# Performance work log

Hardware: AMD Instinct MI355X
Metric: run time of the kernel (lower is better)

Reference implementation:

```python
import jax, jax.numpy as jnp
import numpy as np

N = 100_000   # nodes
E = 1_600_000 # message-passing edges
EA = 1_000_000 # aux edges for bilinear head
G = 512       # graphs in batch
F_IN = 16     # num_node_features (fixed in source)
H = 32        # hidden_dim (fixed in source)


def setup_inputs() -> dict:
    key = jax.random.key(0)
    ks = jax.random.split(key, 8)
    x = jax.random.normal(ks[0], (N, F_IN), jnp.float32)
    edge_index = jax.random.randint(ks[1], (2, E), 0, N, dtype=jnp.int32)
    edge_index_aux = jax.random.randint(ks[2], (2, EA), 0, N, dtype=jnp.int32)
    batch = jnp.sort(jax.random.randint(ks[3], (N,), 0, G, dtype=jnp.int32))
    W1 = jax.random.normal(ks[4], (F_IN, H), jnp.float32) / np.sqrt(F_IN)
    b1 = jnp.zeros((H,), jnp.float32)
    W2 = jax.random.normal(ks[5], (H, H), jnp.float32) / np.sqrt(H)
    b2 = jnp.zeros((H,), jnp.float32)
    Wr = jax.random.normal(ks[6], (H, 1), jnp.float32) / np.sqrt(H)
    br = jnp.zeros((1,), jnp.float32)
    Wbil = jax.random.normal(ks[7], (1, H, H), jnp.float32) / H
    bbil = jnp.zeros((1,), jnp.float32)
    return dict(x=x, edge_index=edge_index, edge_index_aux=edge_index_aux,
                batch=batch, W1=W1, b1=b1, W2=W2, b2=b2, Wr=Wr, br=br,
                Wbil=Wbil, bbil=bbil)


def gcn_conv(x, W, b, src, dst):
    # PyG GCNConv: x' = D^{-1/2}(A+I)D^{-1/2} (x W) + b, deg includes self-loop
    xw = x @ W                                                   # [N,H]
    deg = jax.ops.segment_sum(jnp.ones((src.shape[0],), x.dtype), dst,
                              num_segments=N) + 1.0              # +1 self-loop
    dinv = jax.lax.rsqrt(deg)                                    # [N]
    coef = dinv[src] * dinv[dst]                                 # [E]
    agg = jax.ops.segment_sum(xw[src] * coef[:, None], dst, num_segments=N)
    agg = agg + xw * (dinv * dinv)[:, None]                      # self-loop msg
    return agg + b


def reference(x, edge_index, edge_index_aux, batch,
              W1, b1, W2, b2, Wr, br, Wbil, bbil):
    src, dst = edge_index[0], edge_index[1]
    h = jax.nn.relu(gcn_conv(x, W1, b1, src, dst))
    h = gcn_conv(h, W2, b2, src, dst)
    # global_mean_pool over graph ids
    cnt = jax.ops.segment_sum(jnp.ones((N,), h.dtype), batch, num_segments=G)
    pooled = jax.ops.segment_sum(h, batch, num_segments=G) / jnp.maximum(cnt, 1.0)[:, None]
    reg_output = pooled @ Wr + br                                # [G,1]
    # Bilinear edge head: out_e = x1_e^T W x2_e + b
    h1 = h[edge_index_aux[0]]                                    # [EA,H]
    h2 = h[edge_index_aux[1]]                                    # [EA,H]
    edge_pred = jnp.einsum('ei,ij,ej->e', h1, Wbil[0], h2)[:, None] + bbil
    return reg_output, edge_pred
```

## Files before the change

kernel.cpp:

```cpp
#include <hip/hip_runtime.h>
#include <hip/hip_bf16.h>
#include <string.h>
#include <stdint.h>

typedef __hip_bfloat16 bf16;

#define FIN 16
#define H   32
#define PADW 64
#define NB  512
#define BINCAP 4096
#define NPBMAX 200
#define PSTRIDE 65
#define CHUNK 8192
#define SCAN_CHUNK 1024
#define MAXSEG 64
#define POOLBLK 256

__device__ __forceinline__ float b2f(bf16 v) { return __bfloat162float(v); }

__device__ __forceinline__ float loadf(const void* p, size_t i, int f32) {
    return f32 ? ((const float*)p)[i] : b2f(((const bf16*)p)[i]);
}
__device__ __forceinline__ void storef(void* p, size_t i, float v, int f32) {
    if (f32) ((float*)p)[i] = v;
    else     ((bf16*)p)[i] = __float2bfloat16(v);
}

__device__ __forceinline__ unsigned pack2(float lo, float hi) {
    bf16 a = __float2bfloat16(lo), b = __float2bfloat16(hi);
    unsigned short ua, ub;
    memcpy(&ua, &a, 2); memcpy(&ub, &b, 2);
    return ((unsigned)ub << 16) | (unsigned)ua;
}
__device__ __forceinline__ float f_lo(unsigned u) {
    union { unsigned i; float f; } v; v.i = u << 16; return v.f;
}
__device__ __forceinline__ float f_hi(unsigned u) {
    union { unsigned i; float f; } v; v.i = u & 0xffff0000u; return v.f;
}

__global__ void k_detect(const void* __restrict__ x, int nelem, int* __restrict__ flag,
                         float* __restrict__ zf, int nzf,
                         int* __restrict__ zi, int nzi) {
    for (int i = threadIdx.x; i < nzf; i += blockDim.x) zf[i] = 0.f;
    if (zi) for (int i = threadIdx.x; i < nzi; i += blockDim.x) zi[i] = 0;
    __shared__ int cntS;
    if (threadIdx.x == 0) cntS = 0;
    __syncthreads();
    int bad = 0;
    const bf16* p = (const bf16*)x;
    for (int i = threadIdx.x; i < nelem; i += blockDim.x) {
        float v = b2f(p[i]);
        float a = fabsf(v);
        if (isnan(v) || a > 1024.f || (v != 0.f && a < 1e-20f)) bad++;
    }
    atomicAdd(&cntS, bad);
    __syncthreads();
    if (threadIdx.x == 0) flag[0] = (cntS > 64) ? 1 : 0;
}

__global__ void __launch_bounds__(1024) k_p1(
        const int* __restrict__ src, const int* __restrict__ dst,
        int* __restrict__ bincur, unsigned* __restrict__ binbuf,
        int E, int npb) {
    __shared__ int hcnt[4][NB];
    __shared__ int hbase[NB];
    __shared__ int scur[NB];
    int tid = threadIdx.x;
    int grp = tid >> 8;
    int e0 = blockIdx.x * CHUNK;
    int nE = E - e0;
    if (nE > CHUNK) nE = CHUNK;
    for (int i = tid; i < 4 * NB; i += blockDim.x) ((int*)hcnt)[i] = 0;
    __syncthreads();
    for (int i = tid; i < nE; i += blockDim.x)
        atomicAdd(&hcnt[grp][dst[e0 + i] / npb], 1);
    __syncthreads();
    for (int i = tid; i < NB; i += blockDim.x) {
        int c = hcnt[0][i] + hcnt[1][i] + hcnt[2][i] + hcnt[3][i];
        hbase[i] = c ? atomicAdd(&bincur[i], c) : 0;
        scur[i] = 0;
    }
    __syncthreads();
    for (int i = tid; i < nE; i += blockDim.x) {
        int d = dst[e0 + i];
        int bin = d / npb;
        int pos = hbase[bin] + atomicAdd(&scur[bin], 1);
        if (pos < BINCAP)
            binbuf[(size_t)bin * BINCAP + pos] =
                ((unsigned)src[e0 + i] << 10) | (unsigned)(d - bin * npb);
    }
}

__global__ void __launch_bounds__(256) k_p2(
        const int* __restrict__ bincur, const unsigned* __restrict__ binbuf,
        int* __restrict__ csr, int* __restrict__ deg, float* __restrict__ dinv,
        int N, int npb) {
    __shared__ int cur[NPBMAX];
    __shared__ int psr[NPBMAX * PSTRIDE];
    int b = blockIdx.x;
    int base = b * npb;
    int nn = N - base;
    if (nn > npb) nn = npb;
    if (nn < 0) nn = 0;
    for (int i = threadIdx.x; i < nn; i += blockDim.x) cur[i] = 0;
    __syncthreads();
    int cnt = bincur[b];
    if (cnt > BINCAP) cnt = BINCAP;
    const unsigned* buf = binbuf + (size_t)b * BINCAP;
    for (int j = threadIdx.x; j < cnt; j += blockDim.x) {
        unsigned p = buf[j];
        int loc = (int)(p & 1023u);
        int s = (int)(p >> 10);
        int pos = atomicAdd(&cur[loc], 1);
        if (pos < PADW) psr[loc * PSTRIDE + pos] = s;
    }
    __syncthreads();
    int tot = nn * PADW;
    for (int idx = threadIdx.x; idx < tot; idx += blockDim.x) {
        int i = idx >> 6, p = idx & 63;
        int dg = cur[i];
        if (dg > PADW) dg = PADW;
        if (p < dg)
            csr[((size_t)(base + i) << 6) + p] = psr[i * PSTRIDE + p];
    }
    for (int i = threadIdx.x; i < nn; i += blockDim.x) {
        int dg = cur[i];
        deg[base + i] = dg;
        dinv[base + i] = rsqrtf((float)dg + 1.0f);
    }
}


__global__ void k_fillp(const int* __restrict__ src, const int* __restrict__ dst,
                        int* __restrict__ cursor, int* __restrict__ csr, int E) {
    int e = blockIdx.x * blockDim.x + threadIdx.x;
    if (e >= E) return;
    int d = dst[e];
    int pos = atomicAdd(&cursor[d], 1);
    if (pos < PADW) csr[((size_t)d << 6) + pos] = src[e];
}

__global__ void k_dinvi(const int* __restrict__ deg, float* __restrict__ dinv, int N) {
    int t = blockIdx.x * blockDim.x + threadIdx.x;
    if (t < N) dinv[t] = rsqrtf((float)deg[t] + 1.0f);
}

__global__ void k_gatherpb(const int* __restrict__ deg, const int* __restrict__ csr,
                           const float* __restrict__ dinv, const unsigned* __restrict__ xsb,
                           float2* __restrict__ agg, int N) {
    int t = blockIdx.x * blockDim.x + threadIdx.x;
    int d = t >> 4, j = t & 15;
    if (d >= N) return;
    int len = deg[d];
    if (len > PADW) len = PADW;
    const int* lst = csr + ((size_t)d << 6);
    unsigned u = xsb[(size_t)d * 16 + j];
    float a0 = f_lo(u), a1 = f_hi(u);
    float b0 = 0.f, b1 = 0.f;
    int k = 0;
    for (; k + 4 <= len; k += 4) {
        int4 s4 = *(const int4*)(lst + k);
        unsigned u0 = xsb[(size_t)s4.x * 16 + j];
        unsigned u1 = xsb[(size_t)s4.y * 16 + j];
        unsigned u2 = xsb[(size_t)s4.z * 16 + j];
        unsigned u3 = xsb[(size_t)s4.w * 16 + j];
        a0 += f_lo(u0); a1 += f_hi(u0);
        b0 += f_lo(u1); b1 += f_hi(u1);
        a0 += f_lo(u2); a1 += f_hi(u2);
        b0 += f_lo(u3); b1 += f_hi(u3);
    }
    for (; k < len; k++) {
        unsigned u2 = xsb[(size_t)lst[k] * 16 + j];
        a0 += f_lo(u2); a1 += f_hi(u2);
    }
    float dv = dinv[d];
    agg[(size_t)d * 16 + j] = make_float2((a0 + b0) * dv, (a1 + b1) * dv);
}


__global__ void __launch_bounds__(256) k_xw1v(
        const void* __restrict__ x, const void* __restrict__ W1,
        const float* __restrict__ dinv, const int* __restrict__ flag,
        unsigned* __restrict__ xsb, int N) {
    __shared__ float sW[FIN * H];
    __shared__ float sxx[16 * 17];
    int f32 = flag[0];
    for (int i = threadIdx.x; i < FIN * H; i += blockDim.x) sW[i] = loadf(W1, i, f32);
    __syncthreads();
    int t = blockIdx.x * blockDim.x + threadIdx.x;
    int n = t >> 4, j = t & 15, g = threadIdx.x >> 4;
    if (n < N) sxx[g * 17 + j] = loadf(x, (size_t)n * FIN + j, f32);
    __syncthreads();
    if (n >= N) return;
    float dv = dinv[n];
    float s0 = 0.f, s1 = 0.f;
    const float* xp = &sxx[g * 17];
#pragma unroll
    for (int i = 0; i < FIN; i++) {
        float xv = xp[i];
        s0 += xv * sW[i * H + 2 * j];
        s1 += xv * sW[i * H + 2 * j + 1];
    }
    xsb[(size_t)n * 16 + j] = pack2(s0 * dv, s1 * dv);
}

__global__ void __launch_bounds__(256) k_h1xw2v(
        const void* __restrict__ W2, const void* __restrict__ b1,
        const float* __restrict__ dinv, const int* __restrict__ flag,
        const float2* __restrict__ aggv, unsigned* __restrict__ xsb2, int N) {
    __shared__ float sW[H * H];
    __shared__ float sb[H];
    __shared__ float shh[16 * 33];
    int f32 = flag[0];
    for (int i = threadIdx.x; i < H * H; i += blockDim.x) sW[i] = loadf(W2, i, f32);
    if (threadIdx.x < H) sb[threadIdx.x] = loadf(b1, threadIdx.x, f32);
    __syncthreads();
    int t = blockIdx.x * blockDim.x + threadIdx.x;
    int n = t >> 4, j = t & 15, g = threadIdx.x >> 4;
    if (n < N) {
        float2 a = aggv[(size_t)n * 16 + j];
        float v0 = a.x + sb[2 * j], v1 = a.y + sb[2 * j + 1];
        shh[g * 33 + 2 * j]     = v0 > 0.f ? v0 : 0.f;
        shh[g * 33 + 2 * j + 1] = v1 > 0.f ? v1 : 0.f;
    }
    __syncthreads();
    if (n >= N) return;
    float dv = dinv[n];
    float s0 = 0.f, s1 = 0.f;
    const float* hp = &shh[g * 33];
#pragma unroll
    for (int i = 0; i < H; i++) {
        float hv = hp[i];
        s0 += hv * sW[i * H + 2 * j];
        s1 += hv * sW[i * H + 2 * j + 1];
    }
    xsb2[(size_t)n * 16 + j] = pack2(s0 * dv, s1 * dv);
}

__global__ void __launch_bounds__(512) k_poolhb(
        const void* __restrict__ b2v, const void* __restrict__ Wbil,
        const int* __restrict__ batch, const int* __restrict__ flag,
        const float* __restrict__ aggB, float* __restrict__ pooled,
        float* __restrict__ cnt, bf16* __restrict__ hb, bf16* __restrict__ gb,
        int N) {
    __shared__ float sW[H * H];
    __shared__ float sb[H];
    __shared__ float sh[POOLBLK][H];
    __shared__ int   sg[POOLBLK];
    __shared__ float spool[MAXSEG * H];
    __shared__ float scnt[MAXSEG];
    int f32 = flag[0];
    int tid = threadIdx.x;
    for (int i = tid; i < H * H; i += blockDim.x) sW[i] = loadf(Wbil, i, f32);
    if (tid < H) sb[tid] = loadf(b2v, tid, f32);
    int blk0 = blockIdx.x * POOLBLK;
    int nvalid = N - blk0;
    if (nvalid > POOLBLK) nvalid = POOLBLK;
    if (tid < nvalid) sg[tid] = batch[blk0 + tid];
    for (int i = tid; i < MAXSEG * H; i += blockDim.x) spool[i] = 0.f;
    if (tid < MAXSEG) scnt[tid] = 0.f;
    __syncthreads();
    int f = tid & 31, k = tid >> 5;
    for (int r = k; r < nvalid; r += 16) {
        float v = aggB[(size_t)(blk0 + r) * H + f] + sb[f];
        sh[r][f] = v;
        hb[(size_t)(blk0 + r) * H + f] = __float2bfloat16(v);
    }
    __syncthreads();
    int g0 = sg[0];
    int nseg = sg[nvalid - 1] - g0 + 1;
    if (nseg <= MAXSEG) {
        for (int r = k; r < nvalid; r += 16) {
            int gl = sg[r] - g0;
            atomicAdd(&spool[gl * H + f], sh[r][f]);
            if (f == 0) atomicAdd(&scnt[gl], 1.f);
        }
    } else {
        for (int r = k; r < nvalid; r += 16) {
            atomicAdd(&pooled[(size_t)sg[r] * H + f], sh[r][f]);
            if (f == 0) atomicAdd(&cnt[sg[r]], 1.f);
        }
    }
    for (int r = k; r < nvalid; r += 16) {
        float s = 0.f;
#pragma unroll
        for (int i = 0; i < H; i++) s += sh[r][i] * sW[i * H + f];
        gb[(size_t)(blk0 + r) * H + f] = __float2bfloat16(s);
    }
    if (nseg <= MAXSEG) {
        __syncthreads();
        for (int i = tid; i < nseg * H; i += blockDim.x)
            atomicAdd(&pooled[(size_t)(g0 + (i >> 5)) * H + (i & 31)], spool[i]);
        for (int i = tid; i < nseg; i += blockDim.x)
            atomicAdd(&cnt[g0 + i], scnt[i]);
    }
}


__global__ void k_degi(const int* __restrict__ dst, int* __restrict__ deg, int E) {
    int t = blockIdx.x * blockDim.x + threadIdx.x;
    if (t < E) atomicAdd(&deg[dst[t]], 1);
}

__global__ void k_scan1(const int* __restrict__ deg, int* __restrict__ partials, int N) {
    __shared__ int sd[256];
    int base = blockIdx.x * SCAN_CHUNK + threadIdx.x * 4;
    int s = 0;
#pragma unroll
    for (int k = 0; k < 4; k++) { int i = base + k; s += (i < N) ? deg[i] : 0; }
    sd[threadIdx.x] = s;
    __syncthreads();
    for (int off = 128; off > 0; off >>= 1) {
        if (threadIdx.x < off) sd[threadIdx.x] += sd[threadIdx.x + off];
        __syncthreads();
    }
    if (threadIdx.x == 0) partials[blockIdx.x] = sd[0];
}

__global__ void k_scan2(const int* __restrict__ partials, int* __restrict__ chunk_off, int B1) {
    __shared__ int sd[256];
    int t = threadIdx.x;
    int lv[4];
    int s = 0;
#pragma unroll
    for (int k = 0; k < 4; k++) { int i = t * 4 + k; lv[k] = (i < B1) ? partials[i] : 0; s += lv[k]; }
    sd[t] = s;
    __syncthreads();
    int inc = s;
    for (int off = 1; off < 256; off <<= 1) {
        int v = (t >= off) ? sd[t - off] : 0;
        __syncthreads();
        sd[t] += v;
        __syncthreads();
    }
    int run = sd[t] - inc;
#pragma unroll
    for (int k = 0; k < 4; k++) { int i = t * 4 + k; if (i < B1) chunk_off[i] = run; run += lv[k]; }
    if (t == 255) chunk_off[B1] = run;
}

__global__ void k_scan3(const int* __restrict__ deg, const int* __restrict__ chunk_off,
                        int* __restrict__ row_ptr, int* __restrict__ cursor,
                        int N, int E) {
    __shared__ int sd[256];
    int t = threadIdx.x;
    int base = blockIdx.x * SCAN_CHUNK + t * 4;
    int lv[4];
    int s = 0;
#pragma unroll
    for (int k = 0; k < 4; k++) { int i = base + k; lv[k] = (i < N) ? deg[i] : 0; s += lv[k]; }
    sd[t] = s;
    __syncthreads();
    int inc = s;
    for (int off = 1; off < 256; off <<= 1) {
        int v = (t >= off) ? sd[t - off] : 0;
        __syncthreads();
        sd[t] += v;
        __syncthreads();
    }
    int run = chunk_off[blockIdx.x] + sd[t] - inc;
#pragma unroll
    for (int k = 0; k < 4; k++) {
        int i = base + k;
        if (i < N) { row_ptr[i] = run; cursor[i] = run; }
        run += lv[k];
    }
    if (blockIdx.x == 0 && t == 0) row_ptr[N] = E;
}

__global__ void k_fill(const int* __restrict__ src, const int* __restrict__ dst,
                       int* __restrict__ cursor, int* __restrict__ csr, int E) {
    int e = blockIdx.x * blockDim.x + threadIdx.x;
    if (e >= E) return;
    int pos = atomicAdd(&cursor[dst[e]], 1);
    csr[pos] = src[e];
}

__global__ void k_gather(const int* __restrict__ row_ptr, const int* __restrict__ csr,
                         const float* __restrict__ dinv, const float* __restrict__ xs,
                         float* __restrict__ agg, int N) {
    int t = blockIdx.x * blockDim.x + threadIdx.x;
    int d = t >> 5, f = t & 31;
    if (d >= N) return;
    int beg = row_ptr[d], end = row_ptr[d + 1];
    float acc  = xs[(size_t)d * H + f];
    float acc2 = 0.f;
    int j = beg;
    for (; j + 1 < end; j += 2) {
        int s0 = csr[j], s1 = csr[j + 1];
        acc  += xs[(size_t)s0 * H + f];
        acc2 += xs[(size_t)s1 * H + f];
    }
    if (j < end) acc += xs[(size_t)csr[j] * H + f];
    agg[(size_t)d * H + f] = (acc + acc2) * dinv[d];
}

__global__ void k_xw1n(const void* __restrict__ x, const void* __restrict__ W1,
                       const float* __restrict__ dinv, const int* __restrict__ flag,
                       float* __restrict__ xs, int N) {
    __shared__ float sW[FIN * H];
    int f32 = flag[0];
    for (int i = threadIdx.x; i < FIN * H; i += blockDim.x) sW[i] = loadf(W1, i, f32);
    __syncthreads();
    int n = blockIdx.x * blockDim.x + threadIdx.x;
    if (n >= N) return;
    float xr[FIN];
#pragma unroll
    for (int i = 0; i < FIN; i++) xr[i] = loadf(x, (size_t)n * FIN + i, f32);
    float dv = dinv[n];
#pragma unroll
    for (int f = 0; f < H; f++) {
        float s = 0.f;
#pragma unroll
        for (int i = 0; i < FIN; i++) s += xr[i] * sW[i * H + f];
        xs[(size_t)n * H + f] = s * dv;
    }
}

__global__ void k_h1xw2n(const void* __restrict__ W2, const void* __restrict__ b1,
                         const float* __restrict__ dinv, const int* __restrict__ flag,
                         const float* __restrict__ agg, float* __restrict__ xs2, int N) {
    __shared__ float sW[H * H];
    __shared__ float sb[H];
    int f32 = flag[0];
    for (int i = threadIdx.x; i < H * H; i += blockDim.x) sW[i] = loadf(W2, i, f32);
    if (threadIdx.x < H) sb[threadIdx.x] = loadf(b1, threadIdx.x, f32);
    __syncthreads();
    int n = blockIdx.x * blockDim.x + threadIdx.x;
    if (n >= N) return;
    float hr[H];
#pragma unroll
    for (int f = 0; f < H; f++) {
        float v = agg[(size_t)n * H + f] + sb[f];
        hr[f] = v > 0.f ? v : 0.f;
    }
    float dv = dinv[n];
#pragma unroll
    for (int f = 0; f < H; f++) {
        float s = 0.f;
#pragma unroll
        for (int i = 0; i < H; i++) s += hr[i] * sW[i * H + f];
        xs2[(size_t)n * H + f] = s * dv;
    }
}


__global__ void k_degf(const int* __restrict__ dst, float* __restrict__ deg, int E) {
    int t = blockIdx.x * blockDim.x + threadIdx.x;
    if (t < E) atomicAdd(&deg[dst[t]], 1.0f);
}
__global__ void k_dinvf(float* __restrict__ deg, int N) {
    int t = blockIdx.x * blockDim.x + threadIdx.x;
    if (t < N) deg[t] = rsqrtf(deg[t] + 1.0f);
}
__global__ void k_xw1o(const void* __restrict__ x, const void* __restrict__ W1,
                       const float* __restrict__ dinv, const int* __restrict__ flag,
                       float* __restrict__ xw, float* __restrict__ agg, int N) {
    __shared__ float sW[FIN * H];
    int f32 = flag[0];
    for (int i = threadIdx.x; i < FIN * H; i += blockDim.x) sW[i] = loadf(W1, i, f32);
    __syncthreads();
    int n = blockIdx.x * blockDim.x + threadIdx.x;
    if (n >= N) return;
    float xr[FIN];
#pragma unroll
    for (int i = 0; i < FIN; i++) xr[i] = loadf(x, (size_t)n * FIN + i, f32);
    float dv = dinv[n], dv2 = dv * dv;
#pragma unroll
    for (int f = 0; f < H; f++) {
        float s = 0.f;
#pragma unroll
        for (int i = 0; i < FIN; i++) s += xr[i] * sW[i * H + f];
        xw[(size_t)n * H + f]  = s;
        agg[(size_t)n * H + f] = s * dv2;
    }
}
__global__ void k_scatter(const int* __restrict__ src, const int* __restrict__ dst,
                          const float* __restrict__ dinv, const float* __restrict__ xw,
                          float* __restrict__ agg, int E) {
    int t = blockIdx.x * blockDim.x + threadIdx.x;
    int e = t >> 5, f = t & 31;
    if (e >= E) return;
    int s = src[e], d = dst[e];
    float c = dinv[s] * dinv[d];
    atomicAdd(&agg[(size_t)d * H + f], xw[(size_t)s * H + f] * c);
}
__global__ void k_h1xw2o(const void* __restrict__ W2, const void* __restrict__ b1,
                         const float* __restrict__ dinv, const int* __restrict__ flag,
                         float* __restrict__ aggio, float* __restrict__ xw2, int N) {
    __shared__ float sW[H * H];
    __shared__ float sb[H];
    int f32 = flag[0];
    for (int i = threadIdx.x; i < H * H; i += blockDim.x) sW[i] = loadf(W2, i, f32);
    if (threadIdx.x < H) sb[threadIdx.x] = loadf(b1, threadIdx.x, f32);
    __syncthreads();
    int n = blockIdx.x * blockDim.x + threadIdx.x;
    if (n >= N) return;
    float hr[H];
#pragma unroll
    for (int f = 0; f < H; f++) {
        float v = aggio[(size_t)n * H + f] + sb[f];
        hr[f] = v > 0.f ? v : 0.f;
    }
    float dv = dinv[n], dv2 = dv * dv;
#pragma unroll
    for (int f = 0; f < H; f++) {
        float s = 0.f;
#pragma unroll
        for (int i = 0; i < H; i++) s += hr[i] * sW[i * H + f];
        xw2[(size_t)n * H + f]   = s;
        aggio[(size_t)n * H + f] = s * dv2;
    }
}


__global__ void k_bilreg(const int* __restrict__ srcA, const int* __restrict__ dstA,
                         const unsigned* __restrict__ gb32, const unsigned* __restrict__ hb32,
                         const void* __restrict__ bbil,
                         const float* __restrict__ pooled, const float* __restrict__ cnt,
                         const void* __restrict__ Wr, const void* __restrict__ br,
                         const int* __restrict__ flag, void* __restrict__ out,
                         int G, int EA) {
    int f32 = flag[0];
    int t = blockIdx.x * blockDim.x + threadIdx.x;
    if (t < EA) {
        int s = srcA[t], d = dstA[t];
        const uint4* gp = (const uint4*)(gb32 + (size_t)s * (H / 2));
        const uint4* hp = (const uint4*)(hb32 + (size_t)d * (H / 2));
        float acc = 0.f;
#pragma unroll
        for (int kk = 0; kk < 4; kk++) {
            uint4 a = gp[kk], b = hp[kk];
            acc += f_lo(a.x) * f_lo(b.x) + f_hi(a.x) * f_hi(b.x);
            acc += f_lo(a.y) * f_lo(b.y) + f_hi(a.y) * f_hi(b.y);
            acc += f_lo(a.z) * f_lo(b.z) + f_hi(a.z) * f_hi(b.z);
            acc += f_lo(a.w) * f_lo(b.w) + f_hi(a.w) * f_hi(b.w);
        }
        storef(out, (size_t)G + t, acc + loadf(bbil, 0, f32), f32);
    } else {
        int g = t - EA;
        if (g < G) {
            float c = cnt[g];
            c = c > 1.f ? c : 1.f;
            float s = 0.f;
#pragma unroll
            for (int i = 0; i < H; i++) s += pooled[(size_t)g * H + i] * loadf(Wr, i, f32);
            storef(out, g, s / c + loadf(br, 0, f32), f32);
        }
    }
}

extern "C" void kernel_launch(void* const* d_in, const int* in_sizes, int n_in,
                              void* d_out, int out_size, void* d_ws, size_t ws_size,
                              hipStream_t stream) {
    const void* x     = d_in[0];
    const int*  ei    = (const int*)d_in[1];
    const int*  eia   = (const int*)d_in[2];
    const int*  batch = (const int*)d_in[3];
    const void* W1    = d_in[4];
    const void* b1    = d_in[5];
    const void* W2    = d_in[6];
    const void* b2    = d_in[7];
    const void* Wr    = d_in[8];
    const void* br    = d_in[9];
    const void* Wbil  = d_in[10];
    const void* bbil  = d_in[11];

    const int N  = in_sizes[0] / FIN;
    const int E  = in_sizes[1] / 2;
    const int EA = in_sizes[2] / 2;
    const int G  = out_size - EA;

    float* ws     = (float*)d_ws;
    int*   flag   = (int*)ws;
    float* dinv   = ws + 16;
    float* A      = dinv + N;
    float* B      = A + (size_t)N * H;
    float* pooled = B + (size_t)N * H;
    float* cnt    = pooled + (size_t)G * H;
    float* fend   = cnt + G;

    unsigned* xsb  = (unsigned*)A;
    unsigned* hb32 = (unsigned*)A;
    unsigned* gb32 = hb32 + (size_t)N * (H / 2);

    int* degA   = (int*)fend;
    int* csrA   = (int*)(((uintptr_t)(degA + N) + 15) & ~(uintptr_t)15);
    int* bincur = csrA + (size_t)N * PADW;
    size_t needA  = (size_t)((char*)bincur - (char*)d_ws);
    size_t needA2 = (size_t)((char*)(bincur + NB) - (char*)d_ws);
    const int B1 = (N + SCAN_CHUNK - 1) / SCAN_CHUNK;
    int* deg_i     = (int*)fend;
    int* curB      = deg_i + N;
    int* row_ptr   = curB + N;
    int* chunk_off = row_ptr + N + 1;
    int* csrB      = chunk_off + B1 + 1;
    size_t needB = (size_t)((char*)(csrB + E) - (char*)d_ws);

    const int npb = (N + NB - 1) / NB;
    const bool tierA2 = (ws_size >= needA2) && (npb <= NPBMAX) && (N <= (1 << 22)) &&
                        ((size_t)NB * BINCAP <= (size_t)N * H * 2);
    const bool tierA  = !tierA2 && (ws_size >= needA);
    const bool tierB  = !tierA2 && !tierA && (ws_size >= needB) && (B1 <= 1024);

    const int* src  = ei;
    const int* dst  = ei + E;
    const int* srcA = eia;
    const int* dstA = eia + EA;

    const int TB = 256;
    const int npool = G * H + G;

    k_detect<<<1, 1024, 0, stream>>>(x, 1024, flag, pooled, npool,
                                     tierA2 ? bincur : (int*)nullptr,
                                     tierA2 ? NB : 0);

    int ggrid16 = (int)(((long)N * 16 + TB - 1) / TB);
    int ggrid32 = (int)(((long)N * 32 + TB - 1) / TB);
    int ngrid   = (N + TB - 1) / TB;
    unsigned* xsb2 = xsb;
    float2* aggv = (float2*)B;

    if (tierA2) {
        unsigned* binbuf = (unsigned*)A;
        int nblk1 = (E + CHUNK - 1) / CHUNK;
        k_p1<<<nblk1, 1024, 0, stream>>>(src, dst, bincur, binbuf, E, npb);
        k_p2<<<NB, TB, 0, stream>>>(bincur, binbuf, csrA, degA, dinv, N, npb);
        k_xw1v<<<ggrid16, TB, 0, stream>>>(x, W1, dinv, flag, xsb, N);
        k_gatherpb<<<ggrid16, TB, 0, stream>>>(degA, csrA, dinv, xsb, aggv, N);
        k_h1xw2v<<<ggrid16, TB, 0, stream>>>(W2, b1, dinv, flag, aggv, xsb2, N);
        k_gatherpb<<<ggrid16, TB, 0, stream>>>(degA, csrA, dinv, xsb2, aggv, N);
    } else if (tierA) {
        hipMemsetAsync(degA, 0, (size_t)N * sizeof(int), stream);
        k_fillp<<<(E + TB - 1) / TB, TB, 0, stream>>>(src, dst, degA, csrA, E);
        k_dinvi<<<ngrid, TB, 0, stream>>>(degA, dinv, N);
        k_xw1v<<<ggrid16, TB, 0, stream>>>(x, W1, dinv, flag, xsb, N);
        k_gatherpb<<<ggrid16, TB, 0, stream>>>(degA, csrA, dinv, xsb, aggv, N);
        k_h1xw2v<<<ggrid16, TB, 0, stream>>>(W2, b1, dinv, flag, aggv, xsb2, N);
        k_gatherpb<<<ggrid16, TB, 0, stream>>>(degA, csrA, dinv, xsb2, aggv, N);
    } else if (tierB) {
        hipMemsetAsync(deg_i, 0, (size_t)N * sizeof(int), stream);
        k_degi<<<(E + TB - 1) / TB, TB, 0, stream>>>(dst, deg_i, E);
        k_dinvi<<<ngrid, TB, 0, stream>>>(deg_i, dinv, N);
        k_scan1<<<B1, TB, 0, stream>>>(deg_i, chunk_off, N);
        k_scan2<<<1, TB, 0, stream>>>(chunk_off, chunk_off, B1);
        k_scan3<<<B1, TB, 0, stream>>>(deg_i, chunk_off, row_ptr, curB, N, E);
        k_fill<<<(E + TB - 1) / TB, TB, 0, stream>>>(src, dst, curB, csrB, E);
        k_xw1n<<<ngrid, TB, 0, stream>>>(x, W1, dinv, flag, A, N);
        k_gather<<<ggrid32, TB, 0, stream>>>(row_ptr, csrB, dinv, A, B, N);
        k_h1xw2n<<<ngrid, TB, 0, stream>>>(W2, b1, dinv, flag, B, A, N);
        k_gather<<<ggrid32, TB, 0, stream>>>(row_ptr, csrB, dinv, A, B, N);
    } else {
        hipMemsetAsync(dinv, 0, (size_t)N * sizeof(float), stream);
        k_degf<<<(E + TB - 1) / TB, TB, 0, stream>>>(dst, dinv, E);
        k_dinvf<<<ngrid, TB, 0, stream>>>(dinv, N);
        k_xw1o<<<ngrid, TB, 0, stream>>>(x, W1, dinv, flag, A, B, N);
        long tot = (long)E * 32;
        int sgrid = (int)((tot + TB - 1) / TB);
        k_scatter<<<sgrid, TB, 0, stream>>>(src, dst, dinv, A, B, E);
        k_h1xw2o<<<ngrid, TB, 0, stream>>>(W2, b1, dinv, flag, B, A, N);
        k_scatter<<<sgrid, TB, 0, stream>>>(src, dst, dinv, A, B, E);
    }

    k_poolhb<<<(N + POOLBLK - 1) / POOLBLK, 512, 0, stream>>>(
        b2, Wbil, batch, flag, B, pooled, cnt, (bf16*)hb32, (bf16*)gb32, N);
    k_bilreg<<<(EA + G + TB - 1) / TB, TB, 0, stream>>>(
        srcA, dstA, gb32, hb32, bbil, pooled, cnt, Wr, br, flag, d_out, G, EA);
}
```

Baseline: 274.4 us.

## Fuse XW1 into CSR build and fuse gathers with dense transforms and pooling

```diff
diff --git a/kernel.cpp b/kernel.cpp
--- a/kernel.cpp
+++ b/kernel.cpp
@@ -93,17 +93,22 @@
     }
 }
 
-__global__ void __launch_bounds__(256) k_p2(
+__global__ void __launch_bounds__(256) k_p2x(
         const int* __restrict__ bincur, const unsigned* __restrict__ binbuf,
         int* __restrict__ csr, int* __restrict__ deg, float* __restrict__ dinv,
+        const void* __restrict__ x, const void* __restrict__ W1,
+        const int* __restrict__ flag, unsigned* __restrict__ xsb,
         int N, int npb) {
     __shared__ int cur[NPBMAX];
     __shared__ int psr[NPBMAX * PSTRIDE];
+    __shared__ float sW1[FIN * H];
+    int f32v = flag[0];
     int b = blockIdx.x;
     int base = b * npb;
     int nn = N - base;
     if (nn > npb) nn = npb;
     if (nn < 0) nn = 0;
+    for (int i = threadIdx.x; i < FIN * H; i += blockDim.x) sW1[i] = loadf(W1, i, f32v);
     for (int i = threadIdx.x; i < nn; i += blockDim.x) cur[i] = 0;
     __syncthreads();
     int cnt = bincur[b];
@@ -127,8 +132,43 @@
     }
     for (int i = threadIdx.x; i < nn; i += blockDim.x) {
         int dg = cur[i];
-        deg[base + i] = dg;
-        dinv[base + i] = rsqrtf((float)dg + 1.0f);
+        int n = base + i;
+        deg[n] = dg;
+        float dv = rsqrtf((float)dg + 1.0f);
+        dinv[n] = dv;
+        float xr[FIN];
+        if (f32v) {
+            const float4* xp = (const float4*)((const float*)x + (size_t)n * FIN);
+            float4 v0 = xp[0], v1 = xp[1], v2 = xp[2], v3 = xp[3];
+            xr[0]=v0.x; xr[1]=v0.y; xr[2]=v0.z; xr[3]=v0.w;
+            xr[4]=v1.x; xr[5]=v1.y; xr[6]=v1.z; xr[7]=v1.w;
+            xr[8]=v2.x; xr[9]=v2.y; xr[10]=v2.z; xr[11]=v2.w;
+            xr[12]=v3.x; xr[13]=v3.y; xr[14]=v3.z; xr[15]=v3.w;
+        } else {
+            const uint4* xp = (const uint4*)((const bf16*)x + (size_t)n * FIN);
+            uint4 u0 = xp[0], u1 = xp[1];
+            xr[0]=f_lo(u0.x); xr[1]=f_hi(u0.x); xr[2]=f_lo(u0.y); xr[3]=f_hi(u0.y);
+            xr[4]=f_lo(u0.z); xr[5]=f_hi(u0.z); xr[6]=f_lo(u0.w); xr[7]=f_hi(u0.w);
+            xr[8]=f_lo(u1.x); xr[9]=f_hi(u1.x); xr[10]=f_lo(u1.y); xr[11]=f_hi(u1.y);
+            xr[12]=f_lo(u1.z); xr[13]=f_hi(u1.z); xr[14]=f_lo(u1.w); xr[15]=f_hi(u1.w);
+        }
+        unsigned outp[16];
+#pragma unroll
+        for (int jj = 0; jj < 16; jj++) {
+            float s0 = 0.f, s1 = 0.f;
+#pragma unroll
+            for (int f = 0; f < FIN; f++) {
+                float xv = xr[f];
+                s0 += xv * sW1[f * H + 2 * jj];
+                s1 += xv * sW1[f * H + 2 * jj + 1];
+            }
+            outp[jj] = pack2(s0 * dv, s1 * dv);
+        }
+        uint4* op = (uint4*)(xsb + (size_t)n * 16);
+        op[0] = make_uint4(outp[0], outp[1], outp[2], outp[3]);
+        op[1] = make_uint4(outp[4], outp[5], outp[6], outp[7]);
+        op[2] = make_uint4(outp[8], outp[9], outp[10], outp[11]);
+        op[3] = make_uint4(outp[12], outp[13], outp[14], outp[15]);
     }
 }
 
@@ -147,39 +187,6 @@
     if (t < N) dinv[t] = rsqrtf((float)deg[t] + 1.0f);
 }
 
-__global__ void k_gatherpb(const int* __restrict__ deg, const int* __restrict__ csr,
-                           const float* __restrict__ dinv, const unsigned* __restrict__ xsb,
-                           float2* __restrict__ agg, int N) {
-    int t = blockIdx.x * blockDim.x + threadIdx.x;
-    int d = t >> 4, j = t & 15;
-    if (d >= N) return;
-    int len = deg[d];
-    if (len > PADW) len = PADW;
-    const int* lst = csr + ((size_t)d << 6);
-    unsigned u = xsb[(size_t)d * 16 + j];
-    float a0 = f_lo(u), a1 = f_hi(u);
-    float b0 = 0.f, b1 = 0.f;
-    int k = 0;
-    for (; k + 4 <= len; k += 4) {
-        int4 s4 = *(const int4*)(lst + k);
-        unsigned u0 = xsb[(size_t)s4.x * 16 + j];
-        unsigned u1 = xsb[(size_t)s4.y * 16 + j];
-        unsigned u2 = xsb[(size_t)s4.z * 16 + j];
-        unsigned u3 = xsb[(size_t)s4.w * 16 + j];
-        a0 += f_lo(u0); a1 += f_hi(u0);
-        b0 += f_lo(u1); b1 += f_hi(u1);
-        a0 += f_lo(u2); a1 += f_hi(u2);
-        b0 += f_lo(u3); b1 += f_hi(u3);
-    }
-    for (; k < len; k++) {
-        unsigned u2 = xsb[(size_t)lst[k] * 16 + j];
-        a0 += f_lo(u2); a1 += f_hi(u2);
-    }
-    float dv = dinv[d];
-    agg[(size_t)d * 16 + j] = make_float2((a0 + b0) * dv, (a1 + b1) * dv);
-}
-
-
 __global__ void __launch_bounds__(256) k_xw1v(
         const void* __restrict__ x, const void* __restrict__ W1,
         const float* __restrict__ dinv, const int* __restrict__ flag,
@@ -206,37 +213,153 @@
     xsb[(size_t)n * 16 + j] = pack2(s0 * dv, s1 * dv);
 }
 
-__global__ void __launch_bounds__(256) k_h1xw2v(
+__global__ void __launch_bounds__(256) k_g1(
+        const int* __restrict__ deg, const int* __restrict__ csr,
+        const float* __restrict__ dinv, const unsigned* __restrict__ xsb,
         const void* __restrict__ W2, const void* __restrict__ b1,
-        const float* __restrict__ dinv, const int* __restrict__ flag,
-        const float2* __restrict__ aggv, unsigned* __restrict__ xsb2, int N) {
+        const int* __restrict__ flag, unsigned* __restrict__ xsb2, int N) {
     __shared__ float sW[H * H];
     __shared__ float sb[H];
-    __shared__ float shh[16 * 33];
+    __shared__ float shh[16 * 34];
     int f32 = flag[0];
     for (int i = threadIdx.x; i < H * H; i += blockDim.x) sW[i] = loadf(W2, i, f32);
     if (threadIdx.x < H) sb[threadIdx.x] = loadf(b1, threadIdx.x, f32);
     __syncthreads();
     int t = blockIdx.x * blockDim.x + threadIdx.x;
-    int n = t >> 4, j = t & 15, g = threadIdx.x >> 4;
-    if (n < N) {
-        float2 a = aggv[(size_t)n * 16 + j];
-        float v0 = a.x + sb[2 * j], v1 = a.y + sb[2 * j + 1];
-        shh[g * 33 + 2 * j]     = v0 > 0.f ? v0 : 0.f;
-        shh[g * 33 + 2 * j + 1] = v1 > 0.f ? v1 : 0.f;
-    }
-    __syncthreads();
-    if (n >= N) return;
-    float dv = dinv[n];
+    int d = t >> 4, j = t & 15, g = threadIdx.x >> 4;
+    float dv = 0.f;
+    if (d < N) {
+        int len = deg[d];
+        if (len > PADW) len = PADW;
+        const int* lst = csr + ((size_t)d << 6);
+        unsigned u = xsb[(size_t)d * 16 + j];
+        float a0 = f_lo(u), a1 = f_hi(u);
+        float b0 = 0.f, b1v = 0.f;
+        int k = 0;
+        for (; k + 4 <= len; k += 4) {
+            int4 s4 = *(const int4*)(lst + k);
+            unsigned u0 = xsb[(size_t)s4.x * 16 + j];
+            unsigned u1 = xsb[(size_t)s4.y * 16 + j];
+            unsigned u2 = xsb[(size_t)s4.z * 16 + j];
+            unsigned u3 = xsb[(size_t)s4.w * 16 + j];
+            a0 += f_lo(u0); a1 += f_hi(u0);
+            b0 += f_lo(u1); b1v += f_hi(u1);
+            a0 += f_lo(u2); a1 += f_hi(u2);
+            b0 += f_lo(u3); b1v += f_hi(u3);
+        }
+        for (; k < len; k++) {
+            unsigned u2 = xsb[(size_t)lst[k] * 16 + j];
+            a0 += f_lo(u2); a1 += f_hi(u2);
+        }
+        dv = dinv[d];
+        float h0 = (a0 + b0) * dv + sb[2 * j];
+        float h1 = (a1 + b1v) * dv + sb[2 * j + 1];
+        shh[g * 34 + 2 * j]     = h0 > 0.f ? h0 : 0.f;
+        shh[g * 34 + 2 * j + 1] = h1 > 0.f ? h1 : 0.f;
+    }
+    __syncthreads();
+    if (d >= N) return;
     float s0 = 0.f, s1 = 0.f;
-    const float* hp = &shh[g * 33];
+    const float* hp = &shh[g * 34];
 #pragma unroll
     for (int i = 0; i < H; i++) {
         float hv = hp[i];
         s0 += hv * sW[i * H + 2 * j];
         s1 += hv * sW[i * H + 2 * j + 1];
     }
-    xsb2[(size_t)n * 16 + j] = pack2(s0 * dv, s1 * dv);
+    xsb2[(size_t)d * 16 + j] = pack2(s0 * dv, s1 * dv);
+}
+
+__global__ void __launch_bounds__(256) k_g2(
+        const int* __restrict__ deg, const int* __restrict__ csr,
+        const float* __restrict__ dinv, const unsigned* __restrict__ xsb2,
+        const void* __restrict__ b2v, const void* __restrict__ Wbil,
+        const int* __restrict__ batch, const int* __restrict__ flag,
+        float* __restrict__ pooled, float* __restrict__ cnt,
+        unsigned* __restrict__ hb, unsigned* __restrict__ gb, int N) {
+    __shared__ float sW[H * H];
+    __shared__ float sb[H];
+    __shared__ float shh[16 * 34];
+    __shared__ int   sg[16];
+    __shared__ float spool[16 * H];
+    __shared__ float scnt[16];
+    int f32 = flag[0];
+    int tid = threadIdx.x;
+    for (int i = tid; i < H * H; i += blockDim.x) sW[i] = loadf(Wbil, i, f32);
+    if (tid < H) sb[tid] = loadf(b2v, tid, f32);
+    for (int i = tid; i < 16 * H; i += blockDim.x) spool[i] = 0.f;
+    if (tid < 16) scnt[tid] = 0.f;
+    int blk0 = blockIdx.x * 16;
+    int nv = N - blk0;
+    if (nv > 16) nv = 16;
+    if (tid < nv) sg[tid] = batch[blk0 + tid];
+    __syncthreads();
+    int d = blk0 + (tid >> 4), j = tid & 15, g = tid >> 4;
+    float h0 = 0.f, h1 = 0.f;
+    int valid = (g < nv);
+    if (valid) {
+        int len = deg[d];
+        if (len > PADW) len = PADW;
+        const int* lst = csr + ((size_t)d << 6);
+        unsigned u = xsb2[(size_t)d * 16 + j];
+        float a0 = f_lo(u), a1 = f_hi(u);
+        float b0 = 0.f, b1v = 0.f;
+        int k = 0;
+        for (; k + 4 <= len; k += 4) {
+            int4 s4 = *(const int4*)(lst + k);
+            unsigned u0 = xsb2[(size_t)s4.x * 16 + j];
+            unsigned u1 = xsb2[(size_t)s4.y * 16 + j];
+            unsigned u2 = xsb2[(size_t)s4.z * 16 + j];
+            unsigned u3 = xsb2[(size_t)s4.w * 16 + j];
+            a0 += f_lo(u0); a1 += f_hi(u0);
+            b0 += f_lo(u1); b1v += f_hi(u1);
+            a0 += f_lo(u2); a1 += f_hi(u2);
+            b0 += f_lo(u3); b1v += f_hi(u3);
+        }
+        for (; k < len; k++) {
+            unsigned u2 = xsb2[(size_t)lst[k] * 16 + j];
+            a0 += f_lo(u2); a1 += f_hi(u2);
+        }
+        float dv = dinv[d];
+        h0 = (a0 + b0) * dv + sb[2 * j];
+        h1 = (a1 + b1v) * dv + sb[2 * j + 1];
+        hb[(size_t)d * 16 + j] = pack2(h0, h1);
+        shh[g * 34 + 2 * j]     = h0;
+        shh[g * 34 + 2 * j + 1] = h1;
+    }
+    int g0 = sg[0];
+    int nseg = sg[nv - 1] - g0 + 1;
+    if (valid) {
+        int sgn = sg[g];
+        if (nseg <= 16) {
+            atomicAdd(&spool[(sgn - g0) * H + 2 * j], h0);
+            atomicAdd(&spool[(sgn - g0) * H + 2 * j + 1], h1);
+            if (j == 0) atomicAdd(&scnt[sgn - g0], 1.f);
+        } else {
+            atomicAdd(&pooled[(size_t)sgn * H + 2 * j], h0);
+            atomicAdd(&pooled[(size_t)sgn * H + 2 * j + 1], h1);
+            if (j == 0) atomicAdd(&cnt[sgn], 1.f);
+        }
+    }
+    __syncthreads();
+    if (nseg <= 16) {
+        for (int i = tid; i < nseg * H; i += blockDim.x) {
+            float v = spool[i];
+            if (v != 0.f) atomicAdd(&pooled[(size_t)(g0 + (i >> 5)) * H + (i & 31)], v);
+        }
+        for (int i = tid; i < nseg; i += blockDim.x)
+            if (scnt[i] != 0.f) atomicAdd(&cnt[g0 + i], scnt[i]);
+    }
+    if (!valid) return;
+    float s0 = 0.f, s1 = 0.f;
+    const float* hp = &shh[g * 34];
+#pragma unroll
+    for (int i = 0; i < H; i++) {
+        float hv = hp[i];
+        s0 += hv * sW[i * H + 2 * j];
+        s1 += hv * sW[i * H + 2 * j + 1];
+    }
+    gb[(size_t)d * 16 + j] = pack2(s0, s1);
 }
 
 __global__ void __launch_bounds__(512) k_poolhb(
@@ -582,7 +705,8 @@
     float* cnt    = pooled + (size_t)G * H;
     float* fend   = cnt + G;
 
-    unsigned* xsb  = (unsigned*)A;
+    unsigned* xsb  = (unsigned*)B;
+    unsigned* xsb2 = (unsigned*)B + (size_t)N * 16;
     unsigned* hb32 = (unsigned*)A;
     unsigned* gb32 = hb32 + (size_t)N * (H / 2);
 
@@ -614,32 +738,30 @@
     const int npool = G * H + G;
 
     k_detect<<<1, 1024, 0, stream>>>(x, 1024, flag, pooled, npool,
-                                     tierA2 ? bincur : (int*)nullptr,
+                                     (tierA2 || tierA) ? bincur : (int*)nullptr,
                                      tierA2 ? NB : 0);
 
     int ggrid16 = (int)(((long)N * 16 + TB - 1) / TB);
     int ggrid32 = (int)(((long)N * 32 + TB - 1) / TB);
     int ngrid   = (N + TB - 1) / TB;
-    unsigned* xsb2 = xsb;
-    float2* aggv = (float2*)B;
 
     if (tierA2) {
         unsigned* binbuf = (unsigned*)A;
         int nblk1 = (E + CHUNK - 1) / CHUNK;
         k_p1<<<nblk1, 1024, 0, stream>>>(src, dst, bincur, binbuf, E, npb);
-        k_p2<<<NB, TB, 0, stream>>>(bincur, binbuf, csrA, degA, dinv, N, npb);
-        k_xw1v<<<ggrid16, TB, 0, stream>>>(x, W1, dinv, flag, xsb, N);
-        k_gatherpb<<<ggrid16, TB, 0, stream>>>(degA, csrA, dinv, xsb, aggv, N);
-        k_h1xw2v<<<ggrid16, TB, 0, stream>>>(W2, b1, dinv, flag, aggv, xsb2, N);
-        k_gatherpb<<<ggrid16, TB, 0, stream>>>(degA, csrA, dinv, xsb2, aggv, N);
+        k_p2x<<<NB, TB, 0, stream>>>(bincur, binbuf, csrA, degA, dinv,
+                                     x, W1, flag, xsb, N, npb);
+        k_g1<<<ggrid16, TB, 0, stream>>>(degA, csrA, dinv, xsb, W2, b1, flag, xsb2, N);
+        k_g2<<<ggrid16, TB, 0, stream>>>(degA, csrA, dinv, xsb2, b2, Wbil, batch, flag,
+                                         pooled, cnt, hb32, gb32, N);
     } else if (tierA) {
         hipMemsetAsync(degA, 0, (size_t)N * sizeof(int), stream);
         k_fillp<<<(E + TB - 1) / TB, TB, 0, stream>>>(src, dst, degA, csrA, E);
         k_dinvi<<<ngrid, TB, 0, stream>>>(degA, dinv, N);
         k_xw1v<<<ggrid16, TB, 0, stream>>>(x, W1, dinv, flag, xsb, N);
-        k_gatherpb<<<ggrid16, TB, 0, stream>>>(degA, csrA, dinv, xsb, aggv, N);
-        k_h1xw2v<<<ggrid16, TB, 0, stream>>>(W2, b1, dinv, flag, aggv, xsb2, N);
-        k_gatherpb<<<ggrid16, TB, 0, stream>>>(degA, csrA, dinv, xsb2, aggv, N);
+        k_g1<<<ggrid16, TB, 0, stream>>>(degA, csrA, dinv, xsb, W2, b1, flag, xsb2, N);
+        k_g2<<<ggrid16, TB, 0, stream>>>(degA, csrA, dinv, xsb2, b2, Wbil, batch, flag,
+                                         pooled, cnt, hb32, gb32, N);
     } else if (tierB) {
         hipMemsetAsync(deg_i, 0, (size_t)N * sizeof(int), stream);
         k_degi<<<(E + TB - 1) / TB, TB, 0, stream>>>(dst, deg_i, E);
@@ -652,6 +774,8 @@
         k_gather<<<ggrid32, TB, 0, stream>>>(row_ptr, csrB, dinv, A, B, N);
         k_h1xw2n<<<ngrid, TB, 0, stream>>>(W2, b1, dinv, flag, B, A, N);
         k_gather<<<ggrid32, TB, 0, stream>>>(row_ptr, csrB, dinv, A, B, N);
+        k_poolhb<<<(N + POOLBLK - 1) / POOLBLK, 512, 0, stream>>>(
+            b2, Wbil, batch, flag, B, pooled, cnt, (bf16*)hb32, (bf16*)gb32, N);
     } else {
         hipMemsetAsync(dinv, 0, (size_t)N * sizeof(float), stream);
         k_degf<<<(E + TB - 1) / TB, TB, 0, stream>>>(dst, dinv, E);
@@ -662,10 +786,10 @@
         k_scatter<<<sgrid, TB, 0, stream>>>(src, dst, dinv, A, B, E);
         k_h1xw2o<<<ngrid, TB, 0, stream>>>(W2, b1, dinv, flag, B, A, N);
         k_scatter<<<sgrid, TB, 0, stream>>>(src, dst, dinv, A, B, E);
-    }
-
-    k_poolhb<<<(N + POOLBLK - 1) / POOLBLK, 512, 0, stream>>>(
-        b2, Wbil, batch, flag, B, pooled, cnt, (bf16*)hb32, (bf16*)gb32, N);
+        k_poolhb<<<(N + POOLBLK - 1) / POOLBLK, 512, 0, stream>>>(
+            b2, Wbil, batch, flag, B, pooled, cnt, (bf16*)hb32, (bf16*)gb32, N);
+    }
+
     k_bilreg<<<(EA + G + TB - 1) / TB, TB, 0, stream>>>(
         srcA, dstA, gb32, hb32, bbil, pooled, cnt, Wr, br, flag, d_out, G, EA);
 }
```

Result: faster. 265.1 us (-3.4%).
